# Kernel tuning notes

Measured on AMD Instinct MI355X. Metric: run time of the kernel, lower is better.

Reference implementation:

```python
import jax, jax.numpy as jnp
import numpy as np

N_NODES = 50000
N_EDGES = 800000
D_IN = 256
D_HID = 128


def setup_inputs() -> dict:
    key = jax.random.key(0)
    ks = jax.random.split(key, 10)
    x = jax.random.normal(ks[0], (N_NODES, D_IN), dtype=jnp.float32)
    edge_index = jax.random.randint(ks[1], (2, N_EDGES), 0, N_NODES, dtype=jnp.int64)
    # GCNConv params (glorot-ish init), 3 layers: 256->128, 128->128, 128->128
    def glorot(k, fan_in, fan_out):
        s = jnp.sqrt(6.0 / (fan_in + fan_out))
        return jax.random.uniform(k, (fan_in, fan_out), jnp.float32, -s, s)
    W0 = glorot(ks[2], D_IN, D_HID)
    b0 = jnp.zeros((D_HID,), jnp.float32)
    W1 = glorot(ks[3], D_HID, D_HID)
    b1 = jnp.zeros((D_HID,), jnp.float32)
    W2 = glorot(ks[4], D_HID, D_HID)
    b2 = jnp.zeros((D_HID,), jnp.float32)
    return {"x": x, "edge_index": edge_index, "W0": W0, "b0": b0,
            "W1": W1, "b1": b1, "W2": W2, "b2": b2}


def _gcn_conv(x, W, b, src, dst, deg_inv_sqrt, deg_inv):
    # PyG GCNConv: x' = D^{-1/2} (A + I) D^{-1/2} (x W) + b
    h = x @ W  # [N, d_out]
    norm = deg_inv_sqrt[src] * deg_inv_sqrt[dst]  # [E]
    msg = h[src] * norm[:, None]  # gather + scale, [E, d_out]
    agg = jax.ops.segment_sum(msg, dst, num_segments=x.shape[0])
    # self-loop contribution: norm = deg^{-1/2} * deg^{-1/2} = 1/deg
    return agg + h * deg_inv[:, None] + b


def reference(x, edge_index, W0, b0, W1, b1, W2, b2):
    src, dst = edge_index[0], edge_index[1]
    n = x.shape[0]
    # degree with self loops (computed on destination, source_to_target flow)
    deg = jax.ops.segment_sum(jnp.ones((src.shape[0],), x.dtype), dst,
                              num_segments=n) + 1.0
    deg_inv_sqrt = deg ** -0.5
    deg_inv = 1.0 / deg
    h = jax.nn.relu(_gcn_conv(x, W0, b0, src, dst, deg_inv_sqrt, deg_inv))
    h = jax.nn.relu(_gcn_conv(h, W1, b1, src, dst, deg_inv_sqrt, deg_inv))
    h = jax.nn.relu(_gcn_conv(h, W2, b2, src, dst, deg_inv_sqrt, deg_inv))
    return h
```

## Files before the change

kernel.cpp:

```cpp
#include <hip/hip_runtime.h>

#define N_NODES 50000
#define N_EDGES 800000
#define D_HID   128

typedef unsigned int uint;
typedef unsigned short ushort;
typedef __attribute__((ext_vector_type(8))) short short8;
typedef __attribute__((ext_vector_type(4))) float f32x4;

#define SCAN_NB ((N_NODES + 255) / 256)
#define NB       196
#define CAP      6144
#define P1_BLOCKS 200
#define P1_CHUNK  4000

__global__ __launch_bounds__(256) void part_k(const int* __restrict__ src,
                                              const int* __restrict__ dst,
                                              int* __restrict__ bcur,
                                              int2* __restrict__ ebuf, int e) {
    __shared__ int hist[NB];
    __shared__ int base[NB];
    int tid = threadIdx.x;
    if (tid < NB) hist[tid] = 0;
    __syncthreads();

    int e0 = blockIdx.x * P1_CHUNK;
    int2 ed[16];
    bool val[16];
#pragma unroll
    for (int i = 0; i < 16; ++i) {
        int o = i * 256 + tid;
        int idx = e0 + o;
        val[i] = (o < P1_CHUNK) && (idx < e);
        if (val[i]) {
            ed[i] = make_int2(src[idx], dst[idx]);
            atomicAdd(&hist[ed[i].y >> 8], 1);
        }
    }
    __syncthreads();
    if (tid < NB && hist[tid] > 0) base[tid] = atomicAdd(&bcur[tid], hist[tid]);
    __syncthreads();
    if (tid < NB) hist[tid] = 0;
    __syncthreads();
#pragma unroll
    for (int i = 0; i < 16; ++i) {
        if (val[i]) {
            int bk = ed[i].y >> 8;
            int o  = base[bk] + atomicAdd(&hist[bk], 1);
            if (o < CAP) ebuf[(size_t)bk * CAP + o] = ed[i];
        }
    }
}

__global__ __launch_bounds__(256) void bucket_cnt_k(const int2* __restrict__ ebuf,
                                                    const int* __restrict__ bcnt,
                                                    int* __restrict__ cnt, int n) {
    __shared__ int c[256];
    int b = blockIdx.x, tid = threadIdx.x;
    c[tid] = 0;
    __syncthreads();
    int m = bcnt[b]; if (m > CAP) m = CAP;
    for (int i = tid; i < m; i += 256)
        atomicAdd(&c[ebuf[(size_t)b * CAP + i].y & 255], 1);
    __syncthreads();
    int node = b * 256 + tid;
    if (node < n) cnt[node] = c[tid];
}

__global__ void bsum_k(const int* __restrict__ cnt, int* __restrict__ bsum, int n) {
    int i = blockIdx.x * 256 + threadIdx.x;
    int v = (i < n) ? cnt[i] : 0;
#pragma unroll
    for (int off = 32; off; off >>= 1) v += __shfl_down(v, off, 64);
    __shared__ int ws[4];
    int lane = threadIdx.x & 63, w = threadIdx.x >> 6;
    if (lane == 0) ws[w] = v;
    __syncthreads();
    if (threadIdx.x == 0) bsum[blockIdx.x] = ws[0] + ws[1] + ws[2] + ws[3];
}

__global__ void bscan_k(const int* __restrict__ bsum, int* __restrict__ boff,
                        int* __restrict__ row_ptr_end, int nb) {
    __shared__ int s[256];
    int t = threadIdx.x;
    int v = (t < nb) ? bsum[t] : 0;
    s[t] = v;
    __syncthreads();
    for (int off = 1; off < 256; off <<= 1) {
        int u = (t >= off) ? s[t - off] : 0;
        __syncthreads();
        s[t] += u;
        __syncthreads();
    }
    if (t < nb) boff[t] = s[t] - v;
    if (t == 255) *row_ptr_end = s[255];
}

__global__ void scan3_k(const int* __restrict__ cnt, const int* __restrict__ boff,
                        int* __restrict__ row_ptr, float* __restrict__ dis,
                        float* __restrict__ dinv, int n) {
    __shared__ int s[256];
    int i = blockIdx.x * 256 + threadIdx.x;
    int t = threadIdx.x;
    int v = (i < n) ? cnt[i] : 0;
    s[t] = v;
    __syncthreads();
    for (int off = 1; off < 256; off <<= 1) {
        int u = (t >= off) ? s[t - off] : 0;
        __syncthreads();
        s[t] += u;
        __syncthreads();
    }
    if (i < n) {
        row_ptr[i] = boff[blockIdx.x] + s[t] - v;
        float d = (float)v + 1.0f;
        dis[i]  = rsqrtf(d);
        dinv[i] = 1.0f / d;
    }
}

__global__ __launch_bounds__(256) void csr_k(const int2* __restrict__ ebuf,
                                             const int* __restrict__ bcnt,
                                             const int* __restrict__ row_ptr,
                                             int* __restrict__ col, int n) {
    __shared__ int rp_l[257];
    __shared__ int cur[256];
    __shared__ int win[CAP];
    int b = blockIdx.x, tid = threadIdx.x;
    int node0 = b * 256;
    for (int i = tid; i < 257; i += 256) {
        int nd = node0 + i; if (nd > n) nd = n;
        rp_l[i] = row_ptr[nd];
    }
    cur[tid] = 0;
    __syncthreads();
    int base0 = rp_l[0];
    int m = bcnt[b]; if (m > CAP) m = CAP;

    for (int i = tid; i < m; i += 256) {
        int2 ed = ebuf[(size_t)b * CAP + i];
        int ll = ed.y & 255;
        int pos = rp_l[ll] + atomicAdd(&cur[ll], 1) - base0;
        win[pos] = ed.x;
    }
    __syncthreads();
    for (int i = tid; i < m; i += 256) col[base0 + i] = win[i];
}

__global__ __launch_bounds__(256) void rowsort_k(const int* __restrict__ rp,
                                                 int* __restrict__ col, int n) {
    int node = blockIdx.x * 4 + (threadIdx.x >> 6);
    if (node >= n) return;
    int lane = threadIdx.x & 63;
    int beg = rp[node], end = rp[node + 1];
    int len = end - beg;
    if (len <= 1) return;
    if (len <= 64) {
        int v = (lane < len) ? col[beg + lane] : 0x7fffffff;
#pragma unroll
        for (int k = 2; k <= 64; k <<= 1)
#pragma unroll
            for (int j = k >> 1; j > 0; j >>= 1) {
                int other = __shfl_xor(v, j);
                bool up    = (lane & k) == 0;
                bool small = (lane & j) == 0;
                v = (small == up) ? min(v, other) : max(v, other);
            }
        if (lane < len) col[beg + lane] = v;
    } else if (lane == 0) {
        for (int i = beg + 1; i < end; ++i) {
            int key = col[i]; int j = i - 1;
            while (j >= beg && col[j] > key) { col[j + 1] = col[j]; --j; }
            col[j + 1] = key;
        }
    }
}

__device__ inline ushort f2bf(float f) {
    unsigned u = __float_as_uint(f);
    unsigned rounding = 0x7fffu + ((u >> 16) & 1u);
    return (ushort)((u + rounding) >> 16);
}
__device__ inline float bf_lo(uint v) { return __uint_as_float(v << 16); }
__device__ inline float bf_hi(uint v) { return __uint_as_float(v & 0xffff0000u); }
__device__ inline short8 cvt8(float4 f0, float4 f1) {
    short8 r;
    r[0] = (short)f2bf(f0.x); r[1] = (short)f2bf(f0.y);
    r[2] = (short)f2bf(f0.z); r[3] = (short)f2bf(f0.w);
    r[4] = (short)f2bf(f1.x); r[5] = (short)f2bf(f1.y);
    r[6] = (short)f2bf(f1.z); r[7] = (short)f2bf(f1.w);
    return r;
}

__global__ void wtrans_all_k(const float* __restrict__ W0, const float* __restrict__ W1,
                             const float* __restrict__ W2, ushort* __restrict__ Wt0,
                             ushort* __restrict__ Wt1, ushort* __restrict__ Wt2) {
    int i = blockIdx.x * 256 + threadIdx.x;
    const float* W; ushort* Wt; int K, j;
    if (i < 32768)      { W = W0; Wt = Wt0; K = 256; j = i; }
    else if (i < 49152) { W = W1; Wt = Wt1; K = 128; j = i - 32768; }
    else                { W = W2; Wt = Wt2; K = 128; j = i - 49152; }
    int k = j >> 7, n = j & 127;
    Wt[(size_t)n * K + k] = f2bf(W[j]);
}

template<int K, bool AF32>
__global__ __launch_bounds__(256, 3) void mfma_gemm_k(const void* __restrict__ Ap,
                                                      const ushort* __restrict__ Bt,
                                                      ushort* __restrict__ H,
                                                      int M, int ntiles) {
    constexpr int T   = K / 32;
    constexpr int NC  = (K == 128) ? 4 : 2;
    constexpr int RPT = (K == 128) ? 32 : 16;
    int tid = threadIdx.x;
    int w = tid >> 6, l = tid & 63;
    int lr = l & 15, kg = (l >> 4) * 8;
    int rIn   = (K == 128) ? (w >> 1) * 16 : 0;
    int cBase = (K == 128) ? (w & 1) * 64 : w * 32;

    short8 b[NC][T];
#pragma unroll
    for (int c = 0; c < NC; ++c)
#pragma unroll
        for (int t = 0; t < T; ++t)
            b[c][t] = *(const short8*)&Bt[(size_t)(cBase + c * 16 + lr) * K + t * 32 + kg];

    int tile = blockIdx.x;
    if (tile >= ntiles) return;
    const int G = gridDim.x;

    auto loadA = [&](int tl, short8* dst) {
        int rc = tl * RPT + rIn + lr; if (rc >= M) rc = M - 1;
        if constexpr (AF32) {
            const float* A32 = (const float*)Ap;
#pragma unroll
            for (int t = 0; t < T; ++t) {
                float4 f0 = *(const float4*)&A32[(size_t)rc * K + t * 32 + kg];
                float4 f1 = *(const float4*)&A32[(size_t)rc * K + t * 32 + kg + 4];
                dst[t] = cvt8(f0, f1);
            }
        } else {
            const ushort* A16 = (const ushort*)Ap;
#pragma unroll
            for (int t = 0; t < T; ++t)
                dst[t] = *(const short8*)&A16[(size_t)rc * K + t * 32 + kg];
        }
    };

    short8 a[T];
    loadA(tile, a);
    for (; tile < ntiles; tile += G) {
        short8 an[T];
        int nt = tile + G;
        if (nt < ntiles) loadA(nt, an);

        f32x4 acc[NC];
#pragma unroll
        for (int c = 0; c < NC; ++c) acc[c] = (f32x4){0.f, 0.f, 0.f, 0.f};
#pragma unroll
        for (int t = 0; t < T; ++t)
#pragma unroll
            for (int c = 0; c < NC; ++c)
                acc[c] = __builtin_amdgcn_mfma_f32_16x16x32_bf16(a[t], b[c][t], acc[c], 0, 0, 0);

        int rs = tile * RPT + rIn + (l >> 4) * 4;
#pragma unroll
        for (int c = 0; c < NC; ++c)
#pragma unroll
            for (int j = 0; j < 4; ++j) {
                int r = rs + j;
                if (r < M) H[(size_t)r * 128 + cBase + c * 16 + lr] = f2bf(acc[c][j]);
            }
#pragma unroll
        for (int t = 0; t < T; ++t) a[t] = an[t];
    }
}

template<bool LAST>
__global__ __launch_bounds__(256) void aggregate_k(const ushort* __restrict__ hb,
                                                   const int* __restrict__ row_ptr,
                                                   const int* __restrict__ col,
                                                   const float* __restrict__ dis,
                                                   const float* __restrict__ dinv,
                                                   const float* __restrict__ bias,
                                                   ushort* __restrict__ act,
                                                   float* __restrict__ out, int n) {
    int node = blockIdx.x * 4 + (threadIdx.x >> 6);
    if (node >= n) return;
    int lane = threadIdx.x & 63;
    int g  = lane >> 4;
    int cl = lane & 15;
    const char* base = (const char*)hb + (cl << 4);

    float ax[8];
#pragma unroll
    for (int j = 0; j < 8; ++j) ax[j] = 0.f;

    int beg = row_ptr[node], end = row_ptr[node + 1];
    for (int e = beg; e < end; e += 16) {
        int s[4]; float wv[4];
#pragma unroll
        for (int q = 0; q < 4; ++q) {
            int idx = e + q * 4 + g;
            bool v  = idx < end;
            s[q]  = col[v ? idx : (end - 1)];
            wv[q] = v ? dis[s[q]] : 0.f;
        }
        uint4 u[4];
#pragma unroll
        for (int q = 0; q < 4; ++q)
            u[q] = *(const uint4*)(base + ((size_t)s[q] << 8));
#pragma unroll
        for (int q = 0; q < 4; ++q) {
            float ww = wv[q];
            ax[0] += ww * bf_lo(u[q].x); ax[1] += ww * bf_hi(u[q].x);
            ax[2] += ww * bf_lo(u[q].y); ax[3] += ww * bf_hi(u[q].y);
            ax[4] += ww * bf_lo(u[q].z); ax[5] += ww * bf_hi(u[q].z);
            ax[6] += ww * bf_lo(u[q].w); ax[7] += ww * bf_hi(u[q].w);
        }
    }
#pragma unroll
    for (int j = 0; j < 8; ++j) {
        ax[j] += __shfl_xor(ax[j], 16);
        ax[j] += __shfl_xor(ax[j], 32);
    }
    if (g == 0) {
        float dn = dis[node], di = dinv[node];
        uint4 un = *(const uint4*)(base + ((size_t)node << 8));
        float hs[8] = {bf_lo(un.x), bf_hi(un.x), bf_lo(un.y), bf_hi(un.y),
                       bf_lo(un.z), bf_hi(un.z), bf_lo(un.w), bf_hi(un.w)};
        int c0 = cl * 8;
        float4 bv0 = *(const float4*)&bias[c0];
        float4 bv1 = *(const float4*)&bias[c0 + 4];
        float bb[8] = {bv0.x, bv0.y, bv0.z, bv0.w, bv1.x, bv1.y, bv1.z, bv1.w};
        float o[8];
#pragma unroll
        for (int j = 0; j < 8; ++j)
            o[j] = fmaxf(ax[j] * dn + hs[j] * di + bb[j], 0.f);
        if (LAST) {
            *(float4*)&out[(size_t)node * D_HID + c0]     = make_float4(o[0], o[1], o[2], o[3]);
            *(float4*)&out[(size_t)node * D_HID + c0 + 4] = make_float4(o[4], o[5], o[6], o[7]);
        } else {
            uint4 p;
            p.x = (uint)f2bf(o[0]) | ((uint)f2bf(o[1]) << 16);
            p.y = (uint)f2bf(o[2]) | ((uint)f2bf(o[3]) << 16);
            p.z = (uint)f2bf(o[4]) | ((uint)f2bf(o[5]) << 16);
            p.w = (uint)f2bf(o[6]) | ((uint)f2bf(o[7]) << 16);
            *(uint4*)((char*)act + ((size_t)node << 8) + (cl << 4)) = p;
        }
    }
}

extern "C" void kernel_launch(void* const* d_in, const int* in_sizes, int n_in,
                              void* d_out, int out_size, void* d_ws, size_t ws_size,
                              hipStream_t stream) {
    const float* x  = (const float*)d_in[0];
    const int*   ei = (const int*)d_in[1];
    const float* W0 = (const float*)d_in[2];
    const float* b0 = (const float*)d_in[3];
    const float* W1 = (const float*)d_in[4];
    const float* b1 = (const float*)d_in[5];
    const float* W2 = (const float*)d_in[6];
    const float* b2 = (const float*)d_in[7];
    float* out = (float*)d_out;

    const int N = N_NODES, E = N_EDGES;
    const int* src = ei;
    const int* dst = ei + E;

    char* w = (char*)d_ws;
    size_t off = 0;
    auto alloc = [&](size_t bytes) {
        size_t o = off;
        off += (bytes + 255) & ~(size_t)255;
        return o;
    };
    int*    cnt    = (int*)(w + alloc((size_t)N * 4));
    int*    bcur   = (int*)(w + alloc((size_t)NB * 4));
    float*  dis    = (float*)(w + alloc((size_t)N * 4));
    float*  dinv   = (float*)(w + alloc((size_t)N * 4));
    int*    rp     = (int*)(w + alloc((size_t)(N + 1) * 4));
    int*    bsum   = (int*)(w + alloc((size_t)SCAN_NB * 4));
    int*    boff   = (int*)(w + alloc((size_t)SCAN_NB * 4));
    int*    col    = (int*)(w + alloc((size_t)E * 4));
    int2*   ebuf   = (int2*)(w + alloc((size_t)NB * CAP * 8));
    ushort* hb     = (ushort*)(w + alloc((size_t)N * D_HID * 2));
    ushort* act    = (ushort*)(w + alloc((size_t)N * D_HID * 2));
    ushort* Wt0    = (ushort*)(w + alloc((size_t)128 * 256 * 2));
    ushort* Wt1    = (ushort*)(w + alloc((size_t)128 * 128 * 2));
    ushort* Wt2    = (ushort*)(w + alloc((size_t)128 * 128 * 2));
    (void)ws_size; (void)n_in; (void)in_sizes; (void)out_size;

    hipMemsetAsync(bcur, 0, (size_t)NB * 4, stream);

    part_k<<<P1_BLOCKS, 256, 0, stream>>>(src, dst, bcur, ebuf, E);
    bucket_cnt_k<<<NB, 256, 0, stream>>>(ebuf, bcur, cnt, N);
    bsum_k<<<SCAN_NB, 256, 0, stream>>>(cnt, bsum, N);
    bscan_k<<<1, 256, 0, stream>>>(bsum, boff, rp + N, SCAN_NB);
    scan3_k<<<SCAN_NB, 256, 0, stream>>>(cnt, boff, rp, dis, dinv, N);
    csr_k<<<NB, 256, 0, stream>>>(ebuf, bcur, rp, col, N);
    rowsort_k<<<(N + 3) / 4, 256, 0, stream>>>(rp, col, N);

    wtrans_all_k<<<256, 256, 0, stream>>>(W0, W1, W2, Wt0, Wt1, Wt2);

    const int GG = 768;
    int nt256 = (N + 15) / 16;
    int nt128 = (N + 31) / 32;
    int agg_grid = (N + 3) / 4;

    mfma_gemm_k<256, true><<<GG, 256, 0, stream>>>(x, Wt0, hb, N, nt256);
    aggregate_k<false><<<agg_grid, 256, 0, stream>>>(hb, rp, col, dis, dinv, b0, act, out, N);
    mfma_gemm_k<128, false><<<GG, 256, 0, stream>>>(act, Wt1, hb, N, nt128);
    aggregate_k<false><<<agg_grid, 256, 0, stream>>>(hb, rp, col, dis, dinv, b1, act, out, N);
    mfma_gemm_k<128, false><<<GG, 256, 0, stream>>>(act, Wt2, hb, N, nt128);
    aggregate_k<true><<<agg_grid, 256, 0, stream>>>(hb, rp, col, dis, dinv, b2, act, out, N);
}
```

Before: 235.8 us.

## Prescale GEMM output by deg^-1/2 and drop per-edge weight gathers in aggregation

The GEMM epilogue now multiplies each output row by dis[row], so aggregation sums pre-scaled rows and applies dis[node] once, with the self-loop folded into the same factor. This removes the per-edge dis[src] gather and the dinv array. Out-of-range edge slots now point to a zeroed padding row instead of using a weight mask. The unroll also doubles to 8 edges per group for more memory-level parallelism. The trade-offs are extra bf16 rounding of the scaled values and higher register use.

```diff
diff --git a/kernel.cpp b/kernel.cpp
--- a/kernel.cpp
+++ b/kernel.cpp
@@ -98,8 +98,7 @@
 }
 
 __global__ void scan3_k(const int* __restrict__ cnt, const int* __restrict__ boff,
-                        int* __restrict__ row_ptr, float* __restrict__ dis,
-                        float* __restrict__ dinv, int n) {
+                        int* __restrict__ row_ptr, float* __restrict__ dis, int n) {
     __shared__ int s[256];
     int i = blockIdx.x * 256 + threadIdx.x;
     int t = threadIdx.x;
@@ -114,9 +113,7 @@
     }
     if (i < n) {
         row_ptr[i] = boff[blockIdx.x] + s[t] - v;
-        float d = (float)v + 1.0f;
-        dis[i]  = rsqrtf(d);
-        dinv[i] = 1.0f / d;
+        dis[i] = rsqrtf((float)v + 1.0f);
     }
 }
 
@@ -195,8 +192,10 @@
 
 __global__ void wtrans_all_k(const float* __restrict__ W0, const float* __restrict__ W1,
                              const float* __restrict__ W2, ushort* __restrict__ Wt0,
-                             ushort* __restrict__ Wt1, ushort* __restrict__ Wt2) {
+                             ushort* __restrict__ Wt1, ushort* __restrict__ Wt2,
+                             uint* __restrict__ hb_padrow) {
     int i = blockIdx.x * 256 + threadIdx.x;
+    if (i < 64) hb_padrow[i] = 0;
     const float* W; ushort* Wt; int K, j;
     if (i < 32768)      { W = W0; Wt = Wt0; K = 256; j = i; }
     else if (i < 49152) { W = W1; Wt = Wt1; K = 128; j = i - 32768; }
@@ -208,6 +207,7 @@
 template<int K, bool AF32>
 __global__ __launch_bounds__(256, 3) void mfma_gemm_k(const void* __restrict__ Ap,
                                                       const ushort* __restrict__ Bt,
+                                                      const float* __restrict__ dis,
                                                       ushort* __restrict__ H,
                                                       int M, int ntiles) {
     constexpr int T   = K / 32;
@@ -265,12 +265,15 @@
                 acc[c] = __builtin_amdgcn_mfma_f32_16x16x32_bf16(a[t], b[c][t], acc[c], 0, 0, 0);
 
         int rs = tile * RPT + rIn + (l >> 4) * 4;
+        float dsc[4];
+#pragma unroll
+        for (int j = 0; j < 4; ++j) dsc[j] = (rs + j < M) ? dis[rs + j] : 0.f;
 #pragma unroll
         for (int c = 0; c < NC; ++c)
 #pragma unroll
             for (int j = 0; j < 4; ++j) {
                 int r = rs + j;
-                if (r < M) H[(size_t)r * 128 + cBase + c * 16 + lr] = f2bf(acc[c][j]);
+                if (r < M) H[(size_t)r * 128 + cBase + c * 16 + lr] = f2bf(acc[c][j] * dsc[j]);
             }
 #pragma unroll
         for (int t = 0; t < T; ++t) a[t] = an[t];
@@ -278,11 +281,10 @@
 }
 
 template<bool LAST>
-__global__ __launch_bounds__(256) void aggregate_k(const ushort* __restrict__ hb,
+__global__ __launch_bounds__(256) void aggregate_k(const ushort* __restrict__ hs,
                                                    const int* __restrict__ row_ptr,
                                                    const int* __restrict__ col,
                                                    const float* __restrict__ dis,
-                                                   const float* __restrict__ dinv,
                                                    const float* __restrict__ bias,
                                                    ushort* __restrict__ act,
                                                    float* __restrict__ out, int n) {
@@ -291,33 +293,30 @@
     int lane = threadIdx.x & 63;
     int g  = lane >> 4;
     int cl = lane & 15;
-    const char* base = (const char*)hb + (cl << 4);
+    const char* base = (const char*)hs + (cl << 4);
 
     float ax[8];
 #pragma unroll
     for (int j = 0; j < 8; ++j) ax[j] = 0.f;
 
     int beg = row_ptr[node], end = row_ptr[node + 1];
-    for (int e = beg; e < end; e += 16) {
-        int s[4]; float wv[4];
-#pragma unroll
-        for (int q = 0; q < 4; ++q) {
+    for (int e = beg; e < end; e += 32) {
+        int s[8];
+#pragma unroll
+        for (int q = 0; q < 8; ++q) {
             int idx = e + q * 4 + g;
-            bool v  = idx < end;
-            s[q]  = col[v ? idx : (end - 1)];
-            wv[q] = v ? dis[s[q]] : 0.f;
-        }
-        uint4 u[4];
-#pragma unroll
-        for (int q = 0; q < 4; ++q)
+            s[q] = (idx < end) ? col[idx] : N_NODES;
+        }
+        uint4 u[8];
+#pragma unroll
+        for (int q = 0; q < 8; ++q)
             u[q] = *(const uint4*)(base + ((size_t)s[q] << 8));
 #pragma unroll
-        for (int q = 0; q < 4; ++q) {
-            float ww = wv[q];
-            ax[0] += ww * bf_lo(u[q].x); ax[1] += ww * bf_hi(u[q].x);
-            ax[2] += ww * bf_lo(u[q].y); ax[3] += ww * bf_hi(u[q].y);
-            ax[4] += ww * bf_lo(u[q].z); ax[5] += ww * bf_hi(u[q].z);
-            ax[6] += ww * bf_lo(u[q].w); ax[7] += ww * bf_hi(u[q].w);
+        for (int q = 0; q < 8; ++q) {
+            ax[0] += bf_lo(u[q].x); ax[1] += bf_hi(u[q].x);
+            ax[2] += bf_lo(u[q].y); ax[3] += bf_hi(u[q].y);
+            ax[4] += bf_lo(u[q].z); ax[5] += bf_hi(u[q].z);
+            ax[6] += bf_lo(u[q].w); ax[7] += bf_hi(u[q].w);
         }
     }
 #pragma unroll
@@ -326,10 +325,10 @@
         ax[j] += __shfl_xor(ax[j], 32);
     }
     if (g == 0) {
-        float dn = dis[node], di = dinv[node];
+        float dn = dis[node];
         uint4 un = *(const uint4*)(base + ((size_t)node << 8));
-        float hs[8] = {bf_lo(un.x), bf_hi(un.x), bf_lo(un.y), bf_hi(un.y),
-                       bf_lo(un.z), bf_hi(un.z), bf_lo(un.w), bf_hi(un.w)};
+        float hsn[8] = {bf_lo(un.x), bf_hi(un.x), bf_lo(un.y), bf_hi(un.y),
+                        bf_lo(un.z), bf_hi(un.z), bf_lo(un.w), bf_hi(un.w)};
         int c0 = cl * 8;
         float4 bv0 = *(const float4*)&bias[c0];
         float4 bv1 = *(const float4*)&bias[c0 + 4];
@@ -337,7 +336,7 @@
         float o[8];
 #pragma unroll
         for (int j = 0; j < 8; ++j)
-            o[j] = fmaxf(ax[j] * dn + hs[j] * di + bb[j], 0.f);
+            o[j] = fmaxf((ax[j] + hsn[j]) * dn + bb[j], 0.f);
         if (LAST) {
             *(float4*)&out[(size_t)node * D_HID + c0]     = make_float4(o[0], o[1], o[2], o[3]);
             *(float4*)&out[(size_t)node * D_HID + c0 + 4] = make_float4(o[4], o[5], o[6], o[7]);
@@ -379,13 +378,12 @@
     int*    cnt    = (int*)(w + alloc((size_t)N * 4));
     int*    bcur   = (int*)(w + alloc((size_t)NB * 4));
     float*  dis    = (float*)(w + alloc((size_t)N * 4));
-    float*  dinv   = (float*)(w + alloc((size_t)N * 4));
     int*    rp     = (int*)(w + alloc((size_t)(N + 1) * 4));
     int*    bsum   = (int*)(w + alloc((size_t)SCAN_NB * 4));
     int*    boff   = (int*)(w + alloc((size_t)SCAN_NB * 4));
     int*    col    = (int*)(w + alloc((size_t)E * 4));
     int2*   ebuf   = (int2*)(w + alloc((size_t)NB * CAP * 8));
-    ushort* hb     = (ushort*)(w + alloc((size_t)N * D_HID * 2));
+    ushort* hb     = (ushort*)(w + alloc((size_t)(N + 1) * D_HID * 2));
     ushort* act    = (ushort*)(w + alloc((size_t)N * D_HID * 2));
     ushort* Wt0    = (ushort*)(w + alloc((size_t)128 * 256 * 2));
     ushort* Wt1    = (ushort*)(w + alloc((size_t)128 * 128 * 2));
@@ -398,21 +396,22 @@
     bucket_cnt_k<<<NB, 256, 0, stream>>>(ebuf, bcur, cnt, N);
     bsum_k<<<SCAN_NB, 256, 0, stream>>>(cnt, bsum, N);
     bscan_k<<<1, 256, 0, stream>>>(bsum, boff, rp + N, SCAN_NB);
-    scan3_k<<<SCAN_NB, 256, 0, stream>>>(cnt, boff, rp, dis, dinv, N);
+    scan3_k<<<SCAN_NB, 256, 0, stream>>>(cnt, boff, rp, dis, N);
     csr_k<<<NB, 256, 0, stream>>>(ebuf, bcur, rp, col, N);
     rowsort_k<<<(N + 3) / 4, 256, 0, stream>>>(rp, col, N);
 
-    wtrans_all_k<<<256, 256, 0, stream>>>(W0, W1, W2, Wt0, Wt1, Wt2);
+    wtrans_all_k<<<256, 256, 0, stream>>>(W0, W1, W2, Wt0, Wt1, Wt2,
+                                          (uint*)(hb + (size_t)N * D_HID));
 
     const int GG = 768;
     int nt256 = (N + 15) / 16;
     int nt128 = (N + 31) / 32;
     int agg_grid = (N + 3) / 4;
 
-    mfma_gemm_k<256, true><<<GG, 256, 0, stream>>>(x, Wt0, hb, N, nt256);
-    aggregate_k<false><<<agg_grid, 256, 0, stream>>>(hb, rp, col, dis, dinv, b0, act, out, N);
-    mfma_gemm_k<128, false><<<GG, 256, 0, stream>>>(act, Wt1, hb, N, nt128);
-    aggregate_k<false><<<agg_grid, 256, 0, stream>>>(hb, rp, col, dis, dinv, b1, act, out, N);
-    mfma_gemm_k<128, false><<<GG, 256, 0, stream>>>(act, Wt2, hb, N, nt128);
-    aggregate_k<true><<<agg_grid, 256, 0, stream>>>(hb, rp, col, dis, dinv, b2, act, out, N);
-}
+    mfma_gemm_k<256, true><<<GG, 256, 0, stream>>>(x, Wt0, dis, hb, N, nt256);
+    aggregate_k<false><<<agg_grid, 256, 0, stream>>>(hb, rp, col, dis, b0, act, out, N);
+    mfma_gemm_k<128, false><<<GG, 256, 0, stream>>>(act, Wt1, dis, hb, N, nt128);
+    aggregate_k<false><<<agg_grid, 256, 0, stream>>>(hb, rp, col, dis, b1, act, out, N);
+    mfma_gemm_k<128, false><<<GG, 256, 0, stream>>>(act, Wt2, dis, hb, N, nt128);
+    aggregate_k<true><<<agg_grid, 256, 0, stream>>>(hb, rp, col, dis, b2, act, out, N);
+}
```

Result: slower. 260.2 us (+10.3%).
